# Optimization experiments

Hardware: AMD Instinct MI355X
Metric: run time of the kernel (lower is better)

The kernel has to match this reference:

```python
import jax, jax.numpy as jnp
import numpy as np

K, R, KAPPA = 4, 16384, 32
NX, NF, DOUT = 3, 13, 64


def setup_inputs() -> dict:
    key = jax.random.key(0)
    ks = jax.random.split(key, 6)
    X = jax.random.normal(ks[0], (K, R, NX), dtype=jnp.float32)
    F = jax.random.normal(ks[1], (K, R, NF), dtype=jnp.float32)
    N = jax.random.randint(ks[2], (K, R, KAPPA), 0, R, dtype=jnp.int32)
    H = jax.random.normal(ks[3], (DOUT, NX + NF), dtype=jnp.float32) * 0.1
    gamma = jax.random.normal(ks[4], (DOUT, DOUT), dtype=jnp.float32) * 0.1
    gamma_bias = jax.random.normal(ks[5], (DOUT,), dtype=jnp.float32) * 0.1
    return {"X": X, "F": F, "N": N, "H": H, "gamma": gamma, "gamma_bias": gamma_bias}


def reference(X, F, N, H, gamma, gamma_bias):
    # P = [X | F] : [K, R, n]
    P = jnp.concatenate([X, F], axis=2)
    # batched gather (tf.gather batch_dims=1): P_groups[k, r, i, :] = P[k, N[k, r, i], :]
    P_groups = jax.vmap(lambda p, n: p[n])(P, N)  # [K, R, kappa, n]
    # SharedMLP: P_groups @ H^T, then relu (H_activation)
    PHT = jax.nn.relu(jnp.einsum('krin,dn->krid', P_groups, H))
    # component-wise max over neighbors
    PHT_max = jnp.max(PHT, axis=2)  # [K, R, Dout]
    # Dense: (P* Gamma) + bias, then relu (gamma_activation)
    Y = jnp.einsum('krd,de->kre', PHT_max, gamma) + gamma_bias
    return jax.nn.relu(Y)
```

## Files before the change

kernel.cpp:

```cpp
#include <hip/hip_runtime.h>
#include <hip/hip_fp16.h>
#include <math.h>

#define KR 65536
#define KAPPA 32

typedef __attribute__((ext_vector_type(8))) _Float16 f16x8;
typedef __attribute__((ext_vector_type(4))) float f32x4;

static __device__ __forceinline__ unsigned pkmax(unsigned a, unsigned b) {
  unsigned r;
  asm("v_pk_max_f16 %0, %1, %2" : "=v"(r) : "v"(a), "v"(b));
  return r;
}

__global__ __launch_bounds__(256) void q_kernel(
    const float* __restrict__ X, const float* __restrict__ F,
    const float* __restrict__ H, _Float16* __restrict__ Q) {
  __shared__ float Pl[64 * 16];
  const int t = threadIdx.x;
  const int base = blockIdx.x * 64;

  if (t < 192) Pl[(t / 3) * 16 + (t % 3)] = X[(size_t)base * 3 + t];
  for (int j = t; j < 832; j += 256)
    Pl[(j / 13) * 16 + 3 + (j % 13)] = F[(size_t)base * 13 + j];

  const int lane = t & 63, wave = t >> 6;
  const float4 h0 = *(const float4*)(H + lane * 16 + 0);
  const float4 h1 = *(const float4*)(H + lane * 16 + 4);
  const float4 h2 = *(const float4*)(H + lane * 16 + 8);
  const float4 h3 = *(const float4*)(H + lane * 16 + 12);
  __syncthreads();

  #pragma unroll 4
  for (int p = 0; p < 16; ++p) {
    const int lp = wave * 16 + p;
    const float4* pp = (const float4*)(Pl + lp * 16);
    const float4 p0 = pp[0], p1 = pp[1], p2 = pp[2], p3 = pp[3];
    float q = p0.x * h0.x + p0.y * h0.y + p0.z * h0.z + p0.w * h0.w
            + p1.x * h1.x + p1.y * h1.y + p1.z * h1.z + p1.w * h1.w
            + p2.x * h2.x + p2.y * h2.y + p2.z * h2.z + p2.w * h2.w
            + p3.x * h3.x + p3.y * h3.y + p3.z * h3.z + p3.w * h3.w;
    Q[(size_t)(base + lp) * 64 + lane] = (_Float16)q;
  }
}

__global__ __launch_bounds__(256) void gather_gemm_kernel(
    const _Float16* __restrict__ Q, const int* __restrict__ N,
    const float* __restrict__ gamma, const float* __restrict__ gbias,
    float* __restrict__ Y) {
  __shared__ _Float16 Gt[64 * 72];
  __shared__ _Float16 Ml[64 * 72];
  __shared__ float Bl[64];

  const int t = threadIdx.x;
  for (int i = t; i < 1024; i += 256) {
    const float4 gv = ((const float4*)gamma)[i];
    const int d = i >> 4, e0 = (i & 15) * 4;
    Gt[(e0 + 0) * 72 + d] = (_Float16)gv.x;
    Gt[(e0 + 1) * 72 + d] = (_Float16)gv.y;
    Gt[(e0 + 2) * 72 + d] = (_Float16)gv.z;
    Gt[(e0 + 3) * 72 + d] = (_Float16)gv.w;
  }
  if (t < 64) Bl[t] = gbias[t];

  const int b = blockIdx.x;
  const int xcd = b & 7, bi = b >> 3;
  const int k = xcd >> 1, halfsel = xcd & 1;
  const int base = (k * 256 + halfsel * 128 + bi) * 64;

  const int lane = t & 63, wave = t >> 6;
  const int grp = lane >> 3, member = lane & 7;
  const _Float16* Qk = Q + ((size_t)k << 20);

  #pragma unroll
  for (int oct = 0; oct < 2; ++oct) {
    const int p0 = base + wave * 16 + oct * 8;
    const int4 c = ((const int4*)(N + (size_t)p0 * 32))[lane];
    unsigned m0 = 0u, m1 = 0u, m2 = 0u, m3 = 0u;
    #pragma unroll
    for (int jq = 0; jq < 8; ++jq) {
      const int src = (lane & 0x38) + jq;
      const int i0 = __shfl(c.x, src);
      const int i1 = __shfl(c.y, src);
      const int i2 = __shfl(c.z, src);
      const int i3 = __shfl(c.w, src);
      int4 v;
      v = *(const int4*)(Qk + (size_t)i0 * 64 + member * 8);
      m0 = pkmax(m0, v.x); m1 = pkmax(m1, v.y); m2 = pkmax(m2, v.z); m3 = pkmax(m3, v.w);
      v = *(const int4*)(Qk + (size_t)i1 * 64 + member * 8);
      m0 = pkmax(m0, v.x); m1 = pkmax(m1, v.y); m2 = pkmax(m2, v.z); m3 = pkmax(m3, v.w);
      v = *(const int4*)(Qk + (size_t)i2 * 64 + member * 8);
      m0 = pkmax(m0, v.x); m1 = pkmax(m1, v.y); m2 = pkmax(m2, v.z); m3 = pkmax(m3, v.w);
      v = *(const int4*)(Qk + (size_t)i3 * 64 + member * 8);
      m0 = pkmax(m0, v.x); m1 = pkmax(m1, v.y); m2 = pkmax(m2, v.z); m3 = pkmax(m3, v.w);
    }
    int4 mv; mv.x = (int)m0; mv.y = (int)m1; mv.z = (int)m2; mv.w = (int)m3;
    *(int4*)(Ml + (wave * 16 + oct * 8 + grp) * 72 + member * 8) = mv;
  }
  __syncthreads();

  const int ln15 = lane & 15, quad = lane >> 4;
  f32x4 acc[4] = {{0.f,0.f,0.f,0.f},{0.f,0.f,0.f,0.f},{0.f,0.f,0.f,0.f},{0.f,0.f,0.f,0.f}};
  #pragma unroll
  for (int ks = 0; ks < 2; ++ks) {
    const f16x8 af = *(const f16x8*)(Ml + (wave * 16 + ln15) * 72 + ks * 32 + quad * 8);
    #pragma unroll
    for (int nt = 0; nt < 4; ++nt) {
      const f16x8 bf = *(const f16x8*)(Gt + (nt * 16 + ln15) * 72 + ks * 32 + quad * 8);
      acc[nt] = __builtin_amdgcn_mfma_f32_16x16x32_f16(af, bf, acc[nt], 0, 0, 0);
    }
  }

  #pragma unroll
  for (int nt = 0; nt < 4; ++nt) {
    const float bv = Bl[nt * 16 + ln15];
    #pragma unroll
    for (int r = 0; r < 4; ++r) {
      const float y = fmaxf(acc[nt][r] + bv, 0.0f);
      Y[(size_t)(base + wave * 16 + quad * 4 + r) * 64 + nt * 16 + ln15] = y;
    }
  }
}

extern "C" void kernel_launch(void* const* d_in, const int* in_sizes, int n_in,
                              void* d_out, int out_size, void* d_ws, size_t ws_size,
                              hipStream_t stream) {
  const float* X  = (const float*)d_in[0];
  const float* F  = (const float*)d_in[1];
  const int*   N  = (const int*)d_in[2];
  const float* H  = (const float*)d_in[3];
  const float* G  = (const float*)d_in[4];
  const float* Gb = (const float*)d_in[5];
  float* Y = (float*)d_out;
  _Float16* Q = (_Float16*)d_ws;

  q_kernel<<<1024, 256, 0, stream>>>(X, F, H, Q);
  gather_gemm_kernel<<<1024, 256, 0, stream>>>(Q, N, G, Gb, Y);
}
```

Baseline: 103.9 us.

## Halve points per block, read neighbor indices directly, split MFMA tiles across waves

```diff
diff --git a/kernel.cpp b/kernel.cpp
--- a/kernel.cpp
+++ b/kernel.cpp
@@ -50,11 +50,13 @@
     const float* __restrict__ gamma, const float* __restrict__ gbias,
     float* __restrict__ Y) {
   __shared__ _Float16 Gt[64 * 72];
-  __shared__ _Float16 Ml[64 * 72];
+  __shared__ _Float16 Ml[32 * 72];
   __shared__ float Bl[64];
 
   const int t = threadIdx.x;
-  for (int i = t; i < 1024; i += 256) {
+  #pragma unroll
+  for (int ii = 0; ii < 4; ++ii) {
+    const int i = t + ii * 256;
     const float4 gv = ((const float4*)gamma)[i];
     const int d = i >> 4, e0 = (i & 15) * 4;
     Gt[(e0 + 0) * 72 + d] = (_Float16)gv.x;
@@ -67,58 +69,55 @@
   const int b = blockIdx.x;
   const int xcd = b & 7, bi = b >> 3;
   const int k = xcd >> 1, halfsel = xcd & 1;
-  const int base = (k * 256 + halfsel * 128 + bi) * 64;
+  const int base = k * 16384 + (halfsel * 256 + bi) * 32;
 
   const int lane = t & 63, wave = t >> 6;
   const int grp = lane >> 3, member = lane & 7;
   const _Float16* Qk = Q + ((size_t)k << 20);
 
+  const int p0 = base + wave * 8;
+  const int mypt = p0 + grp;
+  const int* nbase = N + (size_t)mypt * KAPPA;
+  unsigned m0 = 0u, m1 = 0u, m2 = 0u, m3 = 0u;
   #pragma unroll
-  for (int oct = 0; oct < 2; ++oct) {
-    const int p0 = base + wave * 16 + oct * 8;
-    const int4 c = ((const int4*)(N + (size_t)p0 * 32))[lane];
-    unsigned m0 = 0u, m1 = 0u, m2 = 0u, m3 = 0u;
-    #pragma unroll
-    for (int jq = 0; jq < 8; ++jq) {
-      const int src = (lane & 0x38) + jq;
-      const int i0 = __shfl(c.x, src);
-      const int i1 = __shfl(c.y, src);
-      const int i2 = __shfl(c.z, src);
-      const int i3 = __shfl(c.w, src);
-      int4 v;
-      v = *(const int4*)(Qk + (size_t)i0 * 64 + member * 8);
-      m0 = pkmax(m0, v.x); m1 = pkmax(m1, v.y); m2 = pkmax(m2, v.z); m3 = pkmax(m3, v.w);
-      v = *(const int4*)(Qk + (size_t)i1 * 64 + member * 8);
-      m0 = pkmax(m0, v.x); m1 = pkmax(m1, v.y); m2 = pkmax(m2, v.z); m3 = pkmax(m3, v.w);
-      v = *(const int4*)(Qk + (size_t)i2 * 64 + member * 8);
-      m0 = pkmax(m0, v.x); m1 = pkmax(m1, v.y); m2 = pkmax(m2, v.z); m3 = pkmax(m3, v.w);
-      v = *(const int4*)(Qk + (size_t)i3 * 64 + member * 8);
-      m0 = pkmax(m0, v.x); m1 = pkmax(m1, v.y); m2 = pkmax(m2, v.z); m3 = pkmax(m3, v.w);
-    }
+  for (int jq = 0; jq < 8; ++jq) {
+    const int4 c = *(const int4*)(nbase + jq * 4);
+    int4 v;
+    v = *(const int4*)(Qk + (size_t)c.x * 64 + member * 8);
+    m0 = pkmax(m0, v.x); m1 = pkmax(m1, v.y); m2 = pkmax(m2, v.z); m3 = pkmax(m3, v.w);
+    v = *(const int4*)(Qk + (size_t)c.y * 64 + member * 8);
+    m0 = pkmax(m0, v.x); m1 = pkmax(m1, v.y); m2 = pkmax(m2, v.z); m3 = pkmax(m3, v.w);
+    v = *(const int4*)(Qk + (size_t)c.z * 64 + member * 8);
+    m0 = pkmax(m0, v.x); m1 = pkmax(m1, v.y); m2 = pkmax(m2, v.z); m3 = pkmax(m3, v.w);
+    v = *(const int4*)(Qk + (size_t)c.w * 64 + member * 8);
+    m0 = pkmax(m0, v.x); m1 = pkmax(m1, v.y); m2 = pkmax(m2, v.z); m3 = pkmax(m3, v.w);
+  }
+  {
     int4 mv; mv.x = (int)m0; mv.y = (int)m1; mv.z = (int)m2; mv.w = (int)m3;
-    *(int4*)(Ml + (wave * 16 + oct * 8 + grp) * 72 + member * 8) = mv;
+    *(int4*)(Ml + (wave * 8 + grp) * 72 + member * 8) = mv;
   }
   __syncthreads();
 
   const int ln15 = lane & 15, quad = lane >> 4;
-  f32x4 acc[4] = {{0.f,0.f,0.f,0.f},{0.f,0.f,0.f,0.f},{0.f,0.f,0.f,0.f},{0.f,0.f,0.f,0.f}};
+  const int rt = wave & 1, ct = wave >> 1;
+  f32x4 acc[2] = {{0.f,0.f,0.f,0.f},{0.f,0.f,0.f,0.f}};
   #pragma unroll
   for (int ks = 0; ks < 2; ++ks) {
-    const f16x8 af = *(const f16x8*)(Ml + (wave * 16 + ln15) * 72 + ks * 32 + quad * 8);
+    const f16x8 af = *(const f16x8*)(Ml + (rt * 16 + ln15) * 72 + ks * 32 + quad * 8);
     #pragma unroll
-    for (int nt = 0; nt < 4; ++nt) {
-      const f16x8 bf = *(const f16x8*)(Gt + (nt * 16 + ln15) * 72 + ks * 32 + quad * 8);
+    for (int nt = 0; nt < 2; ++nt) {
+      const f16x8 bf = *(const f16x8*)(Gt + (ct * 32 + nt * 16 + ln15) * 72 + ks * 32 + quad * 8);
       acc[nt] = __builtin_amdgcn_mfma_f32_16x16x32_f16(af, bf, acc[nt], 0, 0, 0);
     }
   }
 
   #pragma unroll
-  for (int nt = 0; nt < 4; ++nt) {
-    const float bv = Bl[nt * 16 + ln15];
+  for (int nt = 0; nt < 2; ++nt) {
+    const float bv = Bl[ct * 32 + nt * 16 + ln15];
     #pragma unroll
     for (int r = 0; r < 4; ++r) {
       const float y = fmaxf(acc[nt][r] + bv, 0.0f);
-      Y[(size_t)(base + wave * 16 + quad * 4 + r) * 64 + nt * 16 + ln15] = y;
+      Y[(size_t)(base + rt * 16 + quad * 4 + r) * 64 + ct * 32 + nt * 16 + ln15] = y;
     }
   }
 }
@@ -136,5 +135,5 @@
   _Float16* Q = (_Float16*)d_ws;
 
   q_kernel<<<1024, 256, 0, stream>>>(X, F, H, Q);
-  gather_gemm_kernel<<<1024, 256, 0, stream>>>(Q, N, G, Gb, Y);
+  gather_gemm_kernel<<<2048, 256, 0, stream>>>(Q, N, G, Gb, Y);
 }
```

Measured after the change: 99.65 us. 4.1% less time.
